# Kernel tuning notes

Measured on AMD Instinct MI355X. Metric: run time of the kernel, lower is better.

The kernel has to match this reference:

```python
import jax, jax.numpy as jnp
import numpy as np

B, N, IN, HID, OUT = 32, 128, 64, 128, 64
_off = np.ones((N, N)) - np.eye(N)
RECV, SEND = np.where(_off)  # rel_rec one-hot rows -> receiver idx, rel_send -> sender idx
E = N * (N - 1)


def _bn(x, g, b):
    # BatchNorm1d in training mode over flattened (B*M, C), eps=1e-5, biased var
    c = x.shape[-1]
    xf = x.reshape(-1, c)
    m = xf.mean(0)
    v = ((xf - m) ** 2).mean(0)
    return (((xf - m) / jnp.sqrt(v + 1e-5)) * g + b).reshape(x.shape)


def _mlp(x, W1, b1, W2, b2, g, b):
    h = jax.nn.silu(x @ W1 + b1)
    h = jax.nn.silu(h @ W2 + b2)
    return _bn(h, g, b)


def setup_inputs() -> dict:
    key = jax.random.key(0)
    ks = jax.random.split(key, 8)
    p = lambda k, s: jax.random.normal(k, s, dtype=jnp.float32) * 0.05
    return {
        "node_feature": jax.random.normal(ks[0], (B, N, IN), dtype=jnp.float32),
        "nodes_mask": jnp.ones((B, N), dtype=jnp.float32),
        "edges_mask": jnp.ones((B, E), dtype=jnp.float32),
        "eW1": p(ks[1], (2 * IN, HID)), "eb1": jnp.full((HID,), 0.1, jnp.float32),
        "eW2": p(ks[2], (HID, HID)), "eb2": jnp.full((HID,), 0.1, jnp.float32),
        "eg": jnp.ones((HID,), jnp.float32), "ebt": jnp.zeros((HID,), jnp.float32),
        "nW1": p(ks[3], (HID, HID)), "nb1": jnp.full((HID,), 0.1, jnp.float32),
        "nW2": p(ks[4], (HID, HID)), "nb2": jnp.full((HID,), 0.1, jnp.float32),
        "ng": jnp.ones((HID,), jnp.float32), "nbt": jnp.zeros((HID,), jnp.float32),
        "mW1": p(ks[5], (IN + HID, HID)), "mb1": jnp.full((HID,), 0.1, jnp.float32),
        "mW2": p(ks[6], (HID, OUT)), "mb2": jnp.full((OUT,), 0.1, jnp.float32),
        "mg": jnp.ones((OUT,), jnp.float32), "mbt": jnp.zeros((OUT,), jnp.float32),
        "t_nodes": 0, "t_edges": 0,
    }


def reference(node_feature, nodes_mask, edges_mask,
              eW1, eb1, eW2, eb2, eg, ebt,
              nW1, nb1, nW2, nb2, ng, nbt,
              mW1, mb1, mW2, mb2, mg, mbt,
              t_nodes, t_edges):
    # edge_model: rel_send/rel_rec one-hot matmuls == gathers
    senders = node_feature[:, SEND, :]    # [B,E,IN]
    receivers = node_feature[:, RECV, :]  # [B,E,IN]
    ef = jnp.concatenate([senders, receivers], axis=-1)  # [B,E,2*IN]
    # skip_first_edge_type=True, edge_types=2 -> only edge_nn[1], norm=1.0
    em = edges_mask[:, :, None]
    msg = _mlp(ef, eW1, eb1, eW2, eb2, eg, ebt) * em  # [B,E,HID]
    mij = msg / 1.0
    out = mij * em       # attention=False
    mij_m = mij * em
    # node_model: rel_rec.T matmul == scatter-sum over receivers, then / N
    incoming = jnp.zeros((B, N, HID), msg.dtype).at[:, RECV, :].add(out) / N
    incoming = _mlp(incoming, nW1, nb1, nW2, nb2, ng, nbt) * nodes_mask[:, :, None]
    nef = jnp.concatenate([node_feature, incoming], axis=-1)  # [B,N,IN+HID]
    out_node = _mlp(nef, mW1, mb1, mW2, mb2, mg, mbt) * nodes_mask[:, :, None]
    return (out_node, mij_m)
```

## Files before the change

### kernel.cpp

```cpp
#include <hip/hip_runtime.h>
#include <hip/hip_bf16.h>

#define BB    32
#define NNODE 128
#define INF   64
#define HIDF  128
#define OUTF  64
#define EE    (NNODE*(NNODE-1))
#define TILES 127
#define NBLK_EDGE (BB*TILES)
#define ROWS_E 520192.0f
#define ROWS_N 4096.0f
#define OUT0_ELEMS (BB*NNODE*OUTF)

typedef __bf16 bf16_t;
typedef __bf16 bfrag8 __attribute__((ext_vector_type(8)));
typedef float  floatx4 __attribute__((ext_vector_type(4)));

__device__ __forceinline__ float ld_g(const void* p, size_t i, int bf) {
    return bf ? (float)((const bf16_t*)p)[i] : ((const float*)p)[i];
}
__device__ __forceinline__ void st_g(void* p, size_t i, float v, int bf) {
    if (bf) ((bf16_t*)p)[i] = (bf16_t)v; else ((float*)p)[i] = v;
}
__device__ __forceinline__ void* mij_ptr(void* dout, int bf) {
    return bf ? (void*)((bf16_t*)dout + OUT0_ELEMS)
              : (void*)((float*)dout + OUT0_ELEMS);
}
__device__ __forceinline__ float silu_f(float x) {
    x = fminf(fmaxf(x, -60.f), 60.f);
    return x / (1.0f + __expf(-x));
}

__device__ __forceinline__ int swz_col(int row, int col) {
    return col ^ ((row & 15) << 3);
}

__global__ void k_detect(const unsigned int* __restrict__ eg_words,
                         int* __restrict__ flag, float* __restrict__ totE)
{
    if (threadIdx.x == 0) *flag = (eg_words[0] == 0x3F803F80u) ? 1 : 0;
    if (threadIdx.x < 256) totE[threadIdx.x] = 0.f;
}

__global__ __launch_bounds__(256)
void k_prep(const void* __restrict__ W1g, const void* __restrict__ W2g,
            bf16_t* __restrict__ Wt1, bf16_t* __restrict__ Wt2,
            const int* __restrict__ flagp)
{
    const int bf  = *flagp;
    const int idx = blockIdx.x*256 + threadIdx.x;
    const int mat = idx >> 14;
    const int e   = idx & 16383;
    const int k   = e >> 7, n = e & 127;
    const float v = ld_g(mat ? W2g : W1g, e, bf);
    bf16_t* dst = mat ? Wt2 : Wt1;
    dst[n*128 + swz_col(n, k)] = (bf16_t)v;
}

__global__ __launch_bounds__(256, 2)
void k_edge_mlp(const void* __restrict__ nf,
                const bf16_t* __restrict__ Wt1, const void* __restrict__ b1g,
                const bf16_t* __restrict__ Wt2, const void* __restrict__ b2g,
                void* __restrict__ dout, const int* __restrict__ flagp,
                float* __restrict__ totE)
{
    __shared__ __align__(16) bf16_t lA[128*128];
    __shared__ __align__(16) bf16_t lB[128*128];
    __shared__ float sSum[128], sQ[128];
    const int bf  = *flagp;
    void* h2out = mij_ptr(dout, bf);
    const int bx   = blockIdx.x;
    const int bIdx = bx / TILES;
    const int t    = bx - bIdx*TILES;
    const int tid  = threadIdx.x;

    if (tid < 128) { sSum[tid] = 0.f; sQ[tid] = 0.f; }

    {
        const uint4* src = (const uint4*)Wt1;
        uint4* dst = (uint4*)lB;
#pragma unroll
        for (int s = 0; s < 8; ++s) dst[tid + s*256] = src[tid + s*256];
    }
    {
#pragma unroll
        for (int s = 0; s < 8; ++s) {
            const int u = tid + s*256;
            const int m = u >> 4;
            const int c = (u & 15) ^ (m & 15);
            const int eb = t*128 + m;
            const unsigned recv = ((unsigned)eb * 33027u) >> 22;
            const unsigned rr   = (unsigned)eb - recv*127u;
            const unsigned send = rr + (rr >= recv ? 1u : 0u);
            const int node = (c & 8) ? (int)recv : (int)send;
            const int coff = (c & 7) * 8;
            const size_t gi = ((size_t)(bIdx*NNODE + node))*INF + coff;
            if (bf) {
                ((uint4*)lA)[u] = *(const uint4*)((const bf16_t*)nf + gi);
            } else {
                const float4 f0 = *(const float4*)((const float*)nf + gi);
                const float4 f1 = *(const float4*)((const float*)nf + gi + 4);
                bfrag8 v;
                v[0]=(bf16_t)f0.x; v[1]=(bf16_t)f0.y; v[2]=(bf16_t)f0.z; v[3]=(bf16_t)f0.w;
                v[4]=(bf16_t)f1.x; v[5]=(bf16_t)f1.y; v[6]=(bf16_t)f1.z; v[7]=(bf16_t)f1.w;
                *(bfrag8*)(lA + (size_t)u*8) = v;
            }
        }
    }
    __syncthreads();

    const int w  = tid >> 6;
    const int L  = tid & 63;
    const int wr = w >> 1;
    const int wc = w & 1;
    const int q  = L >> 4;
    const int ln = L & 15;

    const floatx4 zero4 = {0.f, 0.f, 0.f, 0.f};
    floatx4 acc[4][4];
#pragma unroll
    for (int mt = 0; mt < 4; ++mt)
#pragma unroll
        for (int nt = 0; nt < 4; ++nt) acc[mt][nt] = zero4;

#pragma unroll
    for (int kk = 0; kk < 128; kk += 32) {
        bfrag8 af[4], bv[4];
#pragma unroll
        for (int mt = 0; mt < 4; ++mt) {
            const int R = wr*64 + mt*16 + ln;
            af[mt] = *(const bfrag8*)(lA + R*128 + swz_col(R, kk + q*8));
        }
#pragma unroll
        for (int nt = 0; nt < 4; ++nt) {
            const int Rb = wc*64 + nt*16 + ln;
            bv[nt] = *(const bfrag8*)(lB + Rb*128 + swz_col(Rb, kk + q*8));
        }
#pragma unroll
        for (int mt = 0; mt < 4; ++mt)
#pragma unroll
            for (int nt = 0; nt < 4; ++nt)
                acc[mt][nt] = __builtin_amdgcn_mfma_f32_16x16x32_bf16(
                    af[mt], bv[nt], acc[mt][nt], 0, 0, 0);
    }
    __syncthreads();

    {
        const uint4* src = (const uint4*)Wt2;
        uint4* dst = (uint4*)lB;
#pragma unroll
        for (int s = 0; s < 8; ++s) dst[tid + s*256] = src[tid + s*256];
    }
#pragma unroll
    for (int nt = 0; nt < 4; ++nt) {
        const int col = wc*64 + nt*16 + ln;
        const float bias = ld_g(b1g, col, bf);
#pragma unroll
        for (int mt = 0; mt < 4; ++mt)
#pragma unroll
            for (int r = 0; r < 4; ++r) {
                const int R = wr*64 + mt*16 + q*4 + r;
                lA[R*128 + swz_col(R, col)] = (bf16_t)silu_f(acc[mt][nt][r] + bias);
            }
    }
    __syncthreads();

#pragma unroll
    for (int mt = 0; mt < 4; ++mt)
#pragma unroll
        for (int nt = 0; nt < 4; ++nt) acc[mt][nt] = zero4;
#pragma unroll
    for (int kk = 0; kk < 128; kk += 32) {
        bfrag8 af[4], bv[4];
#pragma unroll
        for (int mt = 0; mt < 4; ++mt) {
            const int R = wr*64 + mt*16 + ln;
            af[mt] = *(const bfrag8*)(lA + R*128 + swz_col(R, kk + q*8));
        }
#pragma unroll
        for (int nt = 0; nt < 4; ++nt) {
            const int Rb = wc*64 + nt*16 + ln;
            bv[nt] = *(const bfrag8*)(lB + Rb*128 + swz_col(Rb, kk + q*8));
        }
#pragma unroll
        for (int mt = 0; mt < 4; ++mt)
#pragma unroll
            for (int nt = 0; nt < 4; ++nt)
                acc[mt][nt] = __builtin_amdgcn_mfma_f32_16x16x32_bf16(
                    af[mt], bv[nt], acc[mt][nt], 0, 0, 0);
    }
    __syncthreads();

#pragma unroll
    for (int nt = 0; nt < 4; ++nt) {
        const int col = wc*64 + nt*16 + ln;
        const float bias = ld_g(b2g, col, bf);
        float cs = 0.f, cq = 0.f;
#pragma unroll
        for (int mt = 0; mt < 4; ++mt)
#pragma unroll
            for (int r = 0; r < 4; ++r) {
                const int R = wr*64 + mt*16 + q*4 + r;
                const float v = silu_f(acc[mt][nt][r] + bias);
                cs += v; cq += v*v;
                lB[R*128 + swz_col(R, col)] = (bf16_t)v;
            }
        atomicAdd(&sSum[col], cs);
        atomicAdd(&sQ[col], cq);
    }
    __syncthreads();

    {
        const size_t Rbase = ((size_t)bIdx*EE + (size_t)t*128) * 128;
#pragma unroll
        for (int s = 0; s < 8; ++s) {
            const int u = tid + s*256;
            const int m = u >> 4;
            const int c = (u & 15) ^ (m & 15);
            const size_t go = Rbase + (size_t)m*128 + c*8;
            if (bf) {
                *(uint4*)((bf16_t*)h2out + go) = ((const uint4*)lB)[u];
            } else {
                const bfrag8 v = *(const bfrag8*)(lB + (size_t)u*8);
                float4 f0, f1;
                f0.x=(float)v[0]; f0.y=(float)v[1]; f0.z=(float)v[2]; f0.w=(float)v[3];
                f1.x=(float)v[4]; f1.y=(float)v[5]; f1.z=(float)v[6]; f1.w=(float)v[7];
                *(float4*)((float*)h2out + go)     = f0;
                *(float4*)((float*)h2out + go + 4) = f1;
            }
        }
        if (tid < 128) {
            atomicAdd(&totE[tid],       sSum[tid]);
            atomicAdd(&totE[128 + tid], sQ[tid]);
        }
    }
}

__global__ void k_finalize_edge(const float* __restrict__ tot,
                                const void* __restrict__ g,
                                const void* __restrict__ bt,
                                float* __restrict__ ab,
                                const int* __restrict__ flagp)
{
    const int bf = *flagp;
    const int c = threadIdx.x;
    const float m = tot[c] / ROWS_E;
    float v = tot[128 + c] / ROWS_E - m*m;
    v = fmaxf(v, 0.f);
    const float a = ld_g(g, c, bf) * rsqrtf(v + 1e-5f);
    ab[c]       = a;
    ab[128 + c] = ld_g(bt, c, bf) - m*a;
}

__global__ __launch_bounds__(256)
void k_bn_scatter(void* __restrict__ dout,
                  const void* __restrict__ emask,
                  const float* __restrict__ ab,
                  float* __restrict__ inc,
                  const int* __restrict__ flagp)
{
    const int bf = *flagp;
    void* h2 = mij_ptr(dout, bf);
    const int bx = blockIdx.x;
    const int b  = bx >> 7, i = bx & 127;
    const int tid = threadIdx.x;
    const int c = tid & 127, p = tid >> 7;
    const float alpha = ab[c], beta = ab[128 + c];
    const size_t seg = (size_t)b*EE + (size_t)i*127;
    float acc = 0.f;
    for (int e = p; e < 127; e += 2) {
        const size_t idx = (seg + e)*128 + c;
        const float em  = ld_g(emask, seg + e, bf);
        const float msg = (ld_g(h2, idx, bf)*alpha + beta) * em;
        const float outv = msg * em;
        st_g(h2, idx, outv, bf);
        acc += outv;
    }
    __shared__ float sm[128];
    if (p == 1) sm[c] = acc;
    __syncthreads();
    if (p == 0) inc[(size_t)(b*NNODE + i)*HIDF + c] = (acc + sm[c]) * (1.0f/NNODE);
}

__global__ __launch_bounds__(128)
void k_node_mlp(const float* __restrict__ inc,
                const void* __restrict__ W1g, const void* __restrict__ b1g,
                const void* __restrict__ W2g, const void* __restrict__ b2g,
                float* __restrict__ h2n, float* __restrict__ partialN,
                const int* __restrict__ flagp)
{
    const int bf = *flagp;
    __shared__ float x[16][128];
    __shared__ float h[16][128];
    const int bx = blockIdx.x;
    const int tid = threadIdx.x;
    const int r0 = bx*16;
    for (int r = 0; r < 16; ++r) x[r][tid] = inc[(size_t)(r0 + r)*128 + tid];
    __syncthreads();

    float a1[16];
#pragma unroll
    for (int r = 0; r < 16; ++r) a1[r] = 0.f;
    for (int k = 0; k < 128; ++k) {
        const float wv = ld_g(W1g, k*128 + tid, bf);
#pragma unroll
        for (int r = 0; r < 16; ++r) a1[r] += x[r][k]*wv;
    }
    const float bias1 = ld_g(b1g, tid, bf);
#pragma unroll
    for (int r = 0; r < 16; ++r) h[r][tid] = silu_f(a1[r] + bias1);
    __syncthreads();

    float a2[16];
#pragma unroll
    for (int r = 0; r < 16; ++r) a2[r] = 0.f;
    for (int k = 0; k < 128; ++k) {
        const float wv = ld_g(W2g, k*128 + tid, bf);
#pragma unroll
        for (int r = 0; r < 16; ++r) a2[r] += h[r][k]*wv;
    }
    const float bias2 = ld_g(b2g, tid, bf);
    float s = 0.f, sq = 0.f;
#pragma unroll
    for (int r = 0; r < 16; ++r) {
        const float v = silu_f(a2[r] + bias2);
        h2n[(size_t)(r0 + r)*128 + tid] = v;
        s += v; sq += v*v;
    }
    partialN[(size_t)bx*256 + tid]       = s;
    partialN[(size_t)bx*256 + 128 + tid] = sq;
}

__global__ void k_finalize_node(const float* __restrict__ p,
                                const void* __restrict__ g,
                                const void* __restrict__ bt,
                                float* __restrict__ ab,
                                const int* __restrict__ flagp)
{
    const int bf = *flagp;
    const int c = threadIdx.x;
    float s = 0.f, qv = 0.f;
    for (int blk = 0; blk < 256; ++blk) { s += p[blk*256 + c]; qv += p[blk*256 + 128 + c]; }
    const float m = s / ROWS_N;
    float v = qv / ROWS_N - m*m;
    v = fmaxf(v, 0.f);
    const float a = ld_g(g, c, bf) * rsqrtf(v + 1e-5f);
    ab[c]       = a;
    ab[128 + c] = ld_g(bt, c, bf) - m*a;
}

__global__ __launch_bounds__(128)
void k_final_mlp(const void* __restrict__ nf,
                 const float* __restrict__ h2n, const float* __restrict__ abn,
                 const void* __restrict__ nmask,
                 const void* __restrict__ W1g, const void* __restrict__ b1g,
                 const void* __restrict__ W2g, const void* __restrict__ b2g,
                 float* __restrict__ hm, float* __restrict__ partialM,
                 const int* __restrict__ flagp)
{
    const int bf = *flagp;
    __shared__ float x[16][192];
    __shared__ float h[16][128];
    const int bx = blockIdx.x;
    const int tid = threadIdx.x;
    const int r0 = bx*16;
    const float an = abn[tid], bn = abn[128 + tid];
    for (int r = 0; r < 16; ++r) {
        const int row = r0 + r;
        const float mask = ld_g(nmask, row, bf);
        if (tid < 64) x[r][tid] = ld_g(nf, (size_t)row*INF + tid, bf);
        x[r][64 + tid] = (h2n[(size_t)row*128 + tid]*an + bn) * mask;
    }
    __syncthreads();

    float a1[16];
#pragma unroll
    for (int r = 0; r < 16; ++r) a1[r] = 0.f;
    for (int k = 0; k < 192; ++k) {
        const float wv = ld_g(W1g, k*128 + tid, bf);
#pragma unroll
        for (int r = 0; r < 16; ++r) a1[r] += x[r][k]*wv;
    }
    const float bias1 = ld_g(b1g, tid, bf);
#pragma unroll
    for (int r = 0; r < 16; ++r) h[r][tid] = silu_f(a1[r] + bias1);
    __syncthreads();

    if (tid < 64) {
        float a2[16];
#pragma unroll
        for (int r = 0; r < 16; ++r) a2[r] = 0.f;
        for (int k = 0; k < 128; ++k) {
            const float wv = ld_g(W2g, k*64 + tid, bf);
#pragma unroll
            for (int r = 0; r < 16; ++r) a2[r] += h[r][k]*wv;
        }
        const float bias2 = ld_g(b2g, tid, bf);
        float s = 0.f, sq = 0.f;
#pragma unroll
        for (int r = 0; r < 16; ++r) {
            const float v = silu_f(a2[r] + bias2);
            hm[(size_t)(r0 + r)*OUTF + tid] = v;
            s += v; sq += v*v;
        }
        partialM[(size_t)bx*128 + tid]      = s;
        partialM[(size_t)bx*128 + 64 + tid] = sq;
    }
}

__global__ void k_finalize_m(const float* __restrict__ p,
                             const void* __restrict__ g,
                             const void* __restrict__ bt,
                             float* __restrict__ ab,
                             const int* __restrict__ flagp)
{
    const int bf = *flagp;
    const int c = threadIdx.x;
    float s = 0.f, qv = 0.f;
    for (int blk = 0; blk < 256; ++blk) { s += p[blk*128 + c]; qv += p[blk*128 + 64 + c]; }
    const float m = s / ROWS_N;
    float v = qv / ROWS_N - m*m;
    v = fmaxf(v, 0.f);
    const float a = ld_g(g, c, bf) * rsqrtf(v + 1e-5f);
    ab[c]      = a;
    ab[64 + c] = ld_g(bt, c, bf) - m*a;
}

__global__ void k_out_node(const float* __restrict__ hm,
                           const float* __restrict__ abm,
                           const void* __restrict__ nmask,
                           void* __restrict__ dout,
                           const int* __restrict__ flagp)
{
    const int bf = *flagp;
    const int idx = blockIdx.x*256 + threadIdx.x;
    if (idx >= OUT0_ELEMS) return;
    const int c = idx & 63;
    const int row = idx >> 6;
    const float v = (hm[idx]*abm[c] + abm[64 + c]) * ld_g(nmask, row, bf);
    st_g(dout, idx, v, bf);
}

extern "C" void kernel_launch(void* const* d_in, const int* in_sizes, int n_in,
                              void* d_out, int out_size, void* d_ws, size_t ws_size,
                              hipStream_t stream)
{
    const void* nf    = d_in[0];
    const void* nmask = d_in[1];
    const void* emask = d_in[2];
    const void* eW1   = d_in[3];
    const void* eb1   = d_in[4];
    const void* eW2   = d_in[5];
    const void* eb2   = d_in[6];
    const void* eg    = d_in[7];
    const void* ebt   = d_in[8];
    const void* nW1   = d_in[9];
    const void* nb1   = d_in[10];
    const void* nW2   = d_in[11];
    const void* nb2   = d_in[12];
    const void* ng    = d_in[13];
    const void* nbt   = d_in[14];
    const void* mW1   = d_in[15];
    const void* mb1   = d_in[16];
    const void* mW2   = d_in[17];
    const void* mb2   = d_in[18];
    const void* mg    = d_in[19];
    const void* mbt   = d_in[20];

    float* W    = (float*)d_ws;
    int*   flag = (int*)W;
    float* totE = W    + 64;
    float* abE  = totE + 256;
    float* inc  = abE  + 256;
    float* h2n  = inc  + 524288;
    float* pN   = h2n  + 524288;
    float* abN  = pN   + 65536;
    float* hm   = abN  + 256;
    float* pM   = hm   + 262144;
    float* abM  = pM   + 32768;
    bf16_t* Wt1 = (bf16_t*)(abM + 128);
    bf16_t* Wt2 = Wt1 + 16384;

    k_detect<<<dim3(1), dim3(256), 0, stream>>>((const unsigned int*)eg, flag, totE);
    k_prep<<<dim3(128), dim3(256), 0, stream>>>(eW1, eW2, Wt1, Wt2, flag);
    k_edge_mlp<<<dim3(NBLK_EDGE), dim3(256), 0, stream>>>(nf, Wt1, eb1, Wt2, eb2, d_out, flag, totE);
    k_finalize_edge<<<dim3(1), dim3(128), 0, stream>>>(totE, eg, ebt, abE, flag);
    k_bn_scatter<<<dim3(BB*NNODE), dim3(256), 0, stream>>>(d_out, emask, abE, inc, flag);
    k_node_mlp<<<dim3(256), dim3(128), 0, stream>>>(inc, nW1, nb1, nW2, nb2, h2n, pN, flag);
    k_finalize_node<<<dim3(1), dim3(128), 0, stream>>>(pN, ng, nbt, abN, flag);
    k_final_mlp<<<dim3(256), dim3(128), 0, stream>>>(nf, h2n, abN, nmask, mW1, mb1, mW2, mb2, hm, pM, flag);
    k_finalize_m<<<dim3(1), dim3(64), 0, stream>>>(pM, mg, mbt, abM, flag);
    k_out_node<<<dim3(1024), dim3(256), 0, stream>>>(hm, abM, nmask, d_out, flag);
}
```

Before: 748.5 us.

## Read edge MLP weights from global in fragment layout, drop B LDS tile

Weights are pre-packed into MFMA fragment order so each wave loads its B fragments straight from global/L2 instead of staging them in a 32KB LDS tile. This halves LDS use so four blocks can share a CU. The second-layer output is written directly from registers with scalar stores rather than being staged through LDS for coalesced vector writes. The BN-scatter kernel is vectorised to four channels per thread with eight edge lanes, and small loops get unroll pragmas. The risks are uncoalesced 2-byte/4-byte global output stores and repeated L2 traffic for the weights.

```diff
diff --git a/kernel.cpp b/kernel.cpp
--- a/kernel.cpp
+++ b/kernel.cpp
@@ -15,6 +15,7 @@
 
 typedef __bf16 bf16_t;
 typedef __bf16 bfrag8 __attribute__((ext_vector_type(8)));
+typedef __bf16 bfrag4 __attribute__((ext_vector_type(4)));
 typedef float  floatx4 __attribute__((ext_vector_type(4)));
 
 __device__ __forceinline__ float ld_g(const void* p, size_t i, int bf) {
@@ -45,28 +46,29 @@
 
 __global__ __launch_bounds__(256)
 void k_prep(const void* __restrict__ W1g, const void* __restrict__ W2g,
-            bf16_t* __restrict__ Wt1, bf16_t* __restrict__ Wt2,
+            bf16_t* __restrict__ Wf1, bf16_t* __restrict__ Wf2,
             const int* __restrict__ flagp)
 {
     const int bf  = *flagp;
     const int idx = blockIdx.x*256 + threadIdx.x;
     const int mat = idx >> 14;
     const int e   = idx & 16383;
-    const int k   = e >> 7, n = e & 127;
+    const int n   = e & 127, k = e >> 7;
     const float v = ld_g(mat ? W2g : W1g, e, bf);
-    bf16_t* dst = mat ? Wt2 : Wt1;
-    dst[n*128 + swz_col(n, k)] = (bf16_t)v;
-}
-
-__global__ __launch_bounds__(256, 2)
+    const int NB = n >> 4, ln = n & 15;
+    const int ks = k >> 5, q = (k >> 3) & 3, j = k & 7;
+    bf16_t* dst = mat ? Wf2 : Wf1;
+    dst[((((NB*4 + ks)*4 + q)*16 + ln) << 3) + j] = (bf16_t)v;
+}
+
+__global__ __launch_bounds__(256, 4)
 void k_edge_mlp(const void* __restrict__ nf,
-                const bf16_t* __restrict__ Wt1, const void* __restrict__ b1g,
-                const bf16_t* __restrict__ Wt2, const void* __restrict__ b2g,
+                const bf16_t* __restrict__ Wf1, const void* __restrict__ b1g,
+                const bf16_t* __restrict__ Wf2, const void* __restrict__ b2g,
                 void* __restrict__ dout, const int* __restrict__ flagp,
                 float* __restrict__ totE)
 {
     __shared__ __align__(16) bf16_t lA[128*128];
-    __shared__ __align__(16) bf16_t lB[128*128];
     __shared__ float sSum[128], sQ[128];
     const int bf  = *flagp;
     void* h2out = mij_ptr(dout, bf);
@@ -77,12 +79,6 @@
 
     if (tid < 128) { sSum[tid] = 0.f; sQ[tid] = 0.f; }
 
-    {
-        const uint4* src = (const uint4*)Wt1;
-        uint4* dst = (uint4*)lB;
-#pragma unroll
-        for (int s = 0; s < 8; ++s) dst[tid + s*256] = src[tid + s*256];
-    }
     {
 #pragma unroll
         for (int s = 0; s < 8; ++s) {
@@ -125,7 +121,8 @@
         for (int nt = 0; nt < 4; ++nt) acc[mt][nt] = zero4;
 
 #pragma unroll
-    for (int kk = 0; kk < 128; kk += 32) {
+    for (int ks = 0; ks < 4; ++ks) {
+        const int kk = ks*32;
         bfrag8 af[4], bv[4];
 #pragma unroll
         for (int mt = 0; mt < 4; ++mt) {
@@ -133,10 +130,8 @@
             af[mt] = *(const bfrag8*)(lA + R*128 + swz_col(R, kk + q*8));
         }
 #pragma unroll
-        for (int nt = 0; nt < 4; ++nt) {
-            const int Rb = wc*64 + nt*16 + ln;
-            bv[nt] = *(const bfrag8*)(lB + Rb*128 + swz_col(Rb, kk + q*8));
-        }
+        for (int nt = 0; nt < 4; ++nt)
+            bv[nt] = *(const bfrag8*)(Wf1 + ((size_t)((wc*4 + nt)*4 + ks)*64 + L)*8);
 #pragma unroll
         for (int mt = 0; mt < 4; ++mt)
 #pragma unroll
@@ -146,12 +141,6 @@
     }
     __syncthreads();
 
-    {
-        const uint4* src = (const uint4*)Wt2;
-        uint4* dst = (uint4*)lB;
-#pragma unroll
-        for (int s = 0; s < 8; ++s) dst[tid + s*256] = src[tid + s*256];
-    }
 #pragma unroll
     for (int nt = 0; nt < 4; ++nt) {
         const int col = wc*64 + nt*16 + ln;
@@ -171,7 +160,8 @@
 #pragma unroll
         for (int nt = 0; nt < 4; ++nt) acc[mt][nt] = zero4;
 #pragma unroll
-    for (int kk = 0; kk < 128; kk += 32) {
+    for (int ks = 0; ks < 4; ++ks) {
+        const int kk = ks*32;
         bfrag8 af[4], bv[4];
 #pragma unroll
         for (int mt = 0; mt < 4; ++mt) {
@@ -179,10 +169,8 @@
             af[mt] = *(const bfrag8*)(lA + R*128 + swz_col(R, kk + q*8));
         }
 #pragma unroll
-        for (int nt = 0; nt < 4; ++nt) {
-            const int Rb = wc*64 + nt*16 + ln;
-            bv[nt] = *(const bfrag8*)(lB + Rb*128 + swz_col(Rb, kk + q*8));
-        }
+        for (int nt = 0; nt < 4; ++nt)
+            bv[nt] = *(const bfrag8*)(Wf2 + ((size_t)((wc*4 + nt)*4 + ks)*64 + L)*8);
 #pragma unroll
         for (int mt = 0; mt < 4; ++mt)
 #pragma unroll
@@ -190,50 +178,31 @@
                 acc[mt][nt] = __builtin_amdgcn_mfma_f32_16x16x32_bf16(
                     af[mt], bv[nt], acc[mt][nt], 0, 0, 0);
     }
-    __syncthreads();
-
-#pragma unroll
-    for (int nt = 0; nt < 4; ++nt) {
-        const int col = wc*64 + nt*16 + ln;
-        const float bias = ld_g(b2g, col, bf);
-        float cs = 0.f, cq = 0.f;
-#pragma unroll
-        for (int mt = 0; mt < 4; ++mt)
-#pragma unroll
-            for (int r = 0; r < 4; ++r) {
-                const int R = wr*64 + mt*16 + q*4 + r;
-                const float v = silu_f(acc[mt][nt][r] + bias);
-                cs += v; cq += v*v;
-                lB[R*128 + swz_col(R, col)] = (bf16_t)v;
-            }
-        atomicAdd(&sSum[col], cs);
-        atomicAdd(&sQ[col], cq);
-    }
-    __syncthreads();
 
     {
         const size_t Rbase = ((size_t)bIdx*EE + (size_t)t*128) * 128;
 #pragma unroll
-        for (int s = 0; s < 8; ++s) {
-            const int u = tid + s*256;
-            const int m = u >> 4;
-            const int c = (u & 15) ^ (m & 15);
-            const size_t go = Rbase + (size_t)m*128 + c*8;
-            if (bf) {
-                *(uint4*)((bf16_t*)h2out + go) = ((const uint4*)lB)[u];
-            } else {
-                const bfrag8 v = *(const bfrag8*)(lB + (size_t)u*8);
-                float4 f0, f1;
-                f0.x=(float)v[0]; f0.y=(float)v[1]; f0.z=(float)v[2]; f0.w=(float)v[3];
-                f1.x=(float)v[4]; f1.y=(float)v[5]; f1.z=(float)v[6]; f1.w=(float)v[7];
-                *(float4*)((float*)h2out + go)     = f0;
-                *(float4*)((float*)h2out + go + 4) = f1;
-            }
-        }
-        if (tid < 128) {
-            atomicAdd(&totE[tid],       sSum[tid]);
-            atomicAdd(&totE[128 + tid], sQ[tid]);
-        }
+        for (int nt = 0; nt < 4; ++nt) {
+            const int col = wc*64 + nt*16 + ln;
+            const float bias = ld_g(b2g, col, bf);
+            float cs = 0.f, cq = 0.f;
+#pragma unroll
+            for (int mt = 0; mt < 4; ++mt)
+#pragma unroll
+                for (int r = 0; r < 4; ++r) {
+                    const int R = wr*64 + mt*16 + q*4 + r;
+                    const float v = silu_f(acc[mt][nt][r] + bias);
+                    cs += v; cq += v*v;
+                    st_g(h2out, Rbase + (size_t)R*128 + col, v, bf);
+                }
+            atomicAdd(&sSum[col], cs);
+            atomicAdd(&sQ[col], cq);
+        }
+    }
+    __syncthreads();
+    if (tid < 128) {
+        atomicAdd(&totE[tid],       sSum[tid]);
+        atomicAdd(&totE[128 + tid], sQ[tid]);
     }
 }
 
@@ -265,22 +234,46 @@
     const int bx = blockIdx.x;
     const int b  = bx >> 7, i = bx & 127;
     const int tid = threadIdx.x;
-    const int c = tid & 127, p = tid >> 7;
-    const float alpha = ab[c], beta = ab[128 + c];
+    const int cg = tid & 31, p = tid >> 5;
+    const int c0 = cg*4;
+    const float al0 = ab[c0+0], al1 = ab[c0+1], al2 = ab[c0+2], al3 = ab[c0+3];
+    const float be0 = ab[128+c0+0], be1 = ab[128+c0+1], be2 = ab[128+c0+2], be3 = ab[128+c0+3];
     const size_t seg = (size_t)b*EE + (size_t)i*127;
-    float acc = 0.f;
-    for (int e = p; e < 127; e += 2) {
-        const size_t idx = (seg + e)*128 + c;
+    float s0=0.f, s1=0.f, s2=0.f, s3=0.f;
+    for (int e = p; e < 127; e += 8) {
         const float em  = ld_g(emask, seg + e, bf);
-        const float msg = (ld_g(h2, idx, bf)*alpha + beta) * em;
-        const float outv = msg * em;
-        st_g(h2, idx, outv, bf);
-        acc += outv;
-    }
-    __shared__ float sm[128];
-    if (p == 1) sm[c] = acc;
-    __syncthreads();
-    if (p == 0) inc[(size_t)(b*NNODE + i)*HIDF + c] = (acc + sm[c]) * (1.0f/NNODE);
+        const float em2 = em*em;
+        const size_t base = (seg + e)*128 + c0;
+        float v0, v1, v2, v3;
+        if (bf) {
+            const bfrag4 u = *(const bfrag4*)((const bf16_t*)h2 + base);
+            v0 = (float)u[0]; v1 = (float)u[1]; v2 = (float)u[2]; v3 = (float)u[3];
+        } else {
+            const float4 f = *(const float4*)((const float*)h2 + base);
+            v0 = f.x; v1 = f.y; v2 = f.z; v3 = f.w;
+        }
+        v0 = (v0*al0 + be0)*em2;
+        v1 = (v1*al1 + be1)*em2;
+        v2 = (v2*al2 + be2)*em2;
+        v3 = (v3*al3 + be3)*em2;
+        if (bf) {
+            bfrag4 u; u[0]=(bf16_t)v0; u[1]=(bf16_t)v1; u[2]=(bf16_t)v2; u[3]=(bf16_t)v3;
+            *(bfrag4*)((bf16_t*)h2 + base) = u;
+        } else {
+            float4 f; f.x=v0; f.y=v1; f.z=v2; f.w=v3;
+            *(float4*)((float*)h2 + base) = f;
+        }
+        s0 += v0; s1 += v1; s2 += v2; s3 += v3;
+    }
+    __shared__ float sm[8][128];
+    sm[p][c0+0] = s0; sm[p][c0+1] = s1; sm[p][c0+2] = s2; sm[p][c0+3] = s3;
+    __syncthreads();
+    if (tid < 128) {
+        float tsum = 0.f;
+#pragma unroll
+        for (int wk = 0; wk < 8; ++wk) tsum += sm[wk][tid];
+        inc[(size_t)(b*NNODE + i)*HIDF + tid] = tsum * (1.0f/NNODE);
+    }
 }
 
 __global__ __launch_bounds__(128)
@@ -302,6 +295,7 @@
     float a1[16];
 #pragma unroll
     for (int r = 0; r < 16; ++r) a1[r] = 0.f;
+#pragma unroll 4
     for (int k = 0; k < 128; ++k) {
         const float wv = ld_g(W1g, k*128 + tid, bf);
 #pragma unroll
@@ -315,6 +309,7 @@
     float a2[16];
 #pragma unroll
     for (int r = 0; r < 16; ++r) a2[r] = 0.f;
+#pragma unroll 4
     for (int k = 0; k < 128; ++k) {
         const float wv = ld_g(W2g, k*128 + tid, bf);
 #pragma unroll
@@ -341,6 +336,7 @@
     const int bf = *flagp;
     const int c = threadIdx.x;
     float s = 0.f, qv = 0.f;
+#pragma unroll 8
     for (int blk = 0; blk < 256; ++blk) { s += p[blk*256 + c]; qv += p[blk*256 + 128 + c]; }
     const float m = s / ROWS_N;
     float v = qv / ROWS_N - m*m;
@@ -377,6 +373,7 @@
     float a1[16];
 #pragma unroll
     for (int r = 0; r < 16; ++r) a1[r] = 0.f;
+#pragma unroll 4
     for (int k = 0; k < 192; ++k) {
         const float wv = ld_g(W1g, k*128 + tid, bf);
 #pragma unroll
@@ -391,6 +388,7 @@
         float a2[16];
 #pragma unroll
         for (int r = 0; r < 16; ++r) a2[r] = 0.f;
+#pragma unroll 4
         for (int k = 0; k < 128; ++k) {
             const float wv = ld_g(W2g, k*64 + tid, bf);
 #pragma unroll
@@ -418,6 +416,7 @@
     const int bf = *flagp;
     const int c = threadIdx.x;
     float s = 0.f, qv = 0.f;
+#pragma unroll 8
     for (int blk = 0; blk < 256; ++blk) { s += p[blk*128 + c]; qv += p[blk*128 + 64 + c]; }
     const float m = s / ROWS_N;
     float v = qv / ROWS_N - m*m;
@@ -479,12 +478,12 @@
     float* hm   = abN  + 256;
     float* pM   = hm   + 262144;
     float* abM  = pM   + 32768;
-    bf16_t* Wt1 = (bf16_t*)(abM + 128);
-    bf16_t* Wt2 = Wt1 + 16384;
+    bf16_t* Wf1 = (bf16_t*)(abM + 128);
+    bf16_t* Wf2 = Wf1 + 16384;
 
     k_detect<<<dim3(1), dim3(256), 0, stream>>>((const unsigned int*)eg, flag, totE);
-    k_prep<<<dim3(128), dim3(256), 0, stream>>>(eW1, eW2, Wt1, Wt2, flag);
-    k_edge_mlp<<<dim3(NBLK_EDGE), dim3(256), 0, stream>>>(nf, Wt1, eb1, Wt2, eb2, d_out, flag, totE);
+    k_prep<<<dim3(128), dim3(256), 0, stream>>>(eW1, eW2, Wf1, Wf2, flag);
+    k_edge_mlp<<<dim3(NBLK_EDGE), dim3(256), 0, stream>>>(nf, Wf1, eb1, Wf2, eb2, d_out, flag, totE);
     k_finalize_edge<<<dim3(1), dim3(128), 0, stream>>>(totE, eg, ebt, abE, flag);
     k_bn_scatter<<<dim3(BB*NNODE), dim3(256), 0, stream>>>(d_out, emask, abE, inc, flag);
     k_node_mlp<<<dim3(256), dim3(128), 0, stream>>>(inc, nW1, nb1, nW2, nb2, h2n, pN, flag);
```

New measurement: 653.2 us. 1.15x faster.
